# Performance work log

Hardware: AMD Instinct MI355X
Metric: run time of the kernel (lower is better)

The kernel has to match this reference:

```python
import jax, jax.numpy as jnp
import numpy as np


def setup_inputs() -> dict:
    key = jax.random.key(0)
    k1, k2 = jax.random.split(key)
    B, N, V = 8, 64, 128000
    sampled_probs = jax.random.uniform(k1, (B, N, V), dtype=jnp.float32)
    parent_probs = jax.random.uniform(k2, (B, N), dtype=jnp.float32)
    return {
        "sampled_probs": sampled_probs,
        "parent_probs": parent_probs,
        "sample_k": 64,
    }


def reference(sampled_probs, parent_probs, sample_k):
    # sampled_probs: [B, N, V] per-leaf next-token probs
    # parent_probs:  [B, N]    cumulative prob of each leaf (parent path)
    B, N, V = sampled_probs.shape
    # joint path probability: [B, N, V]
    global_probs = sampled_probs * parent_probs[:, :, None]
    # flatten leaves x vocab and take global top-k per batch row
    flattened = global_probs.reshape(B, N * V)
    topk_probs, topk_indices = jax.lax.top_k(flattened, sample_k)  # [B, k]
    # decode flat index -> (parent leaf index, token id)
    parent_indices = (topk_indices // V).astype(jnp.int64)
    token_ids = (topk_indices % V).astype(jnp.int64)
    return token_ids, topk_probs, parent_indices
```

## Files before the change

### kernel.cpp

```cpp
#include <hip/hip_runtime.h>
#include <stdint.h>

#define BATCH 8
#define NLEAF 64
#define VOCAB 128000
#define ROW (NLEAF * VOCAB)
#define CHUNK 4096
#define NCHUNK (ROW / CHUNK)
#define TOPK 64

__global__ __launch_bounds__(256) void k_chunkmax(
    const float* __restrict__ sp, const float* __restrict__ pp,
    float* __restrict__ cmax)
{
    int c   = blockIdx.x;
    int row = c / NCHUNK;
    int cr  = c - row * NCHUNK;
    long base = (long)row * ROW + (long)cr * CHUNK;
    int fr    = cr * CHUNK;
    int leaf0 = fr / VOCAB;
    int bnd   = (leaf0 + 1) * VOCAB;
    float p0  = pp[row * NLEAF + leaf0];
    float p1  = (leaf0 + 1 < NLEAF) ? pp[row * NLEAF + leaf0 + 1] : 0.f;

    int t = threadIdx.x;
    const float4* sp4 = (const float4*)(sp + base);
    float m = 0.f;
#pragma unroll
    for (int i = 0; i < 4; ++i) {
        int e4 = t + i * 256;
        float4 v = sp4[e4];
        float p = ((fr + e4 * 4) < bnd) ? p0 : p1;
        m = fmaxf(m, fmaxf(fmaxf(v.x * p, v.y * p), fmaxf(v.z * p, v.w * p)));
    }
    for (int off = 32; off; off >>= 1) m = fmaxf(m, __shfl_down(m, off, 64));
    __shared__ float s[4];
    if ((t & 63) == 0) s[t >> 6] = m;
    __syncthreads();
    if (t == 0) cmax[c] = fmaxf(fmaxf(s[0], s[1]), fmaxf(s[2], s[3]));
}

__global__ __launch_bounds__(256) void k_threshold(
    const float* __restrict__ cmax, float* __restrict__ thr,
    int* __restrict__ cnt)
{
    int row = blockIdx.x;
    int t = threadIdx.x;
    __shared__ unsigned uv[NCHUNK];
    __shared__ int hist[256], sc[256];
    __shared__ unsigned s_prefix;
    __shared__ int s_k;
    for (int i = t; i < NCHUNK; i += 256)
        uv[i] = __float_as_uint(cmax[row * NCHUNK + i]);
    if (t == 0) { cnt[row] = 0; s_prefix = 0u; s_k = TOPK; }
    __syncthreads();

    for (int level = 3; level >= 0; --level) {
        int shift = level * 8;
        hist[t] = 0;
        __syncthreads();
        unsigned prefix = s_prefix; int kk = s_k;
        for (int i = t; i < NCHUNK; i += 256) {
            unsigned u = uv[i];
            bool mm = (level == 3) || ((u >> (shift + 8)) == prefix);
            unsigned bin = mm ? ((u >> shift) & 255u) : 0xFFFFFFFFu;
            unsigned fb = __builtin_amdgcn_readfirstlane(bin);
            unsigned long long bal = __ballot(bin == fb);
            if (bal == ~0ull) {
                if ((t & 63) == 0 && fb != 0xFFFFFFFFu) atomicAdd(&hist[fb], 64);
            } else if (bin != 0xFFFFFFFFu) {
                atomicAdd(&hist[bin], 1);
            }
        }
        __syncthreads();
        sc[t] = hist[t];
        __syncthreads();
        for (int off = 1; off < 256; off <<= 1) {
            int v = sc[t];
            if (t + off < 256) v += sc[t + off];
            __syncthreads();
            sc[t] = v;
            __syncthreads();
        }
        int gt = (t < 255) ? sc[t + 1] : 0;
        if (gt < kk && kk <= gt + hist[t]) {
            s_prefix = (prefix << 8) | (unsigned)t;
            s_k = kk - gt;
        }
        __syncthreads();
    }
    if (t == 0) thr[row] = __uint_as_float(s_prefix);
}

__global__ __launch_bounds__(256) void k_collect(
    const float* __restrict__ sp, const float* __restrict__ pp,
    const float* __restrict__ cmax, const float* __restrict__ thr,
    int* __restrict__ cnt, unsigned long long* __restrict__ cand, int cap)
{
    int c   = blockIdx.x;
    int row = c / NCHUNK;
    float tval = thr[row];
    if (cmax[c] < tval) return;

    int cr = c - row * NCHUNK;
    long base = (long)row * ROW + (long)cr * CHUNK;
    int fr    = cr * CHUNK;
    int leaf0 = fr / VOCAB;
    int bnd   = (leaf0 + 1) * VOCAB;
    float p0  = pp[row * NLEAF + leaf0];
    float p1  = (leaf0 + 1 < NLEAF) ? pp[row * NLEAF + leaf0 + 1] : 0.f;

    int t = threadIdx.x;
    const float4* sp4 = (const float4*)(sp + base);
    float pr[16];
    int m = 0;
#pragma unroll
    for (int i = 0; i < 4; ++i) {
        int e4 = t + i * 256;
        float4 v = sp4[e4];
        float p = ((fr + e4 * 4) < bnd) ? p0 : p1;
        pr[i * 4 + 0] = v.x * p;
        pr[i * 4 + 1] = v.y * p;
        pr[i * 4 + 2] = v.z * p;
        pr[i * 4 + 3] = v.w * p;
#pragma unroll
        for (int j = 0; j < 4; ++j) m += (pr[i * 4 + j] >= tval) ? 1 : 0;
    }

    __shared__ int sc2[256];
    __shared__ int sbase;
    sc2[t] = m;
    __syncthreads();
    for (int off = 1; off < 256; off <<= 1) {
        int v = sc2[t];
        if (t >= off) v += sc2[t - off];
        __syncthreads();
        sc2[t] = v;
        __syncthreads();
    }
    if (t == 255) sbase = atomicAdd(&cnt[row], sc2[255]);
    __syncthreads();

    if (m > 0) {
        int pos = sbase + sc2[t] - m;
#pragma unroll
        for (int i = 0; i < 4; ++i) {
#pragma unroll
            for (int j = 0; j < 4; ++j) {
                float v = pr[i * 4 + j];
                if (v >= tval) {
                    if (pos < cap) {
                        unsigned fb = __float_as_uint(v);
                        unsigned fi = (unsigned)(fr + (t + i * 256) * 4 + j);
                        cand[(long)row * cap + pos] =
                            ((unsigned long long)fb << 32) |
                            (unsigned long long)(0xFFFFFFFFu - fi);
                    }
                    pos++;
                }
            }
        }
    }
}

__global__ __launch_bounds__(256) void k_final(
    const int* __restrict__ cnt, const unsigned long long* __restrict__ cand,
    int cap, float* __restrict__ out)
{
    int row = blockIdx.x;
    int t = threadIdx.x;
    int nc = cnt[row]; if (nc > cap) nc = cap;
    const unsigned long long* c = cand + (long)row * cap;

    __shared__ int hist[256], sc[256];
    __shared__ unsigned long long s_prefix;
    __shared__ int s_k;
    __shared__ unsigned long long stop[TOPK];
    __shared__ int s_ntop;
    if (t == 0) { s_prefix = 0ull; s_k = TOPK; s_ntop = 0; }
    __syncthreads();

    for (int level = 7; level >= 0; --level) {
        int shift = level * 8;
        hist[t] = 0;
        __syncthreads();
        unsigned long long prefix = s_prefix; int kk = s_k;
        for (int i = t; i < nc; i += 256) {
            unsigned long long u = c[i];
            bool mm = (level == 7) || ((u >> (shift + 8)) == prefix);
            unsigned bin = mm ? (unsigned)((u >> shift) & 255ull) : 0xFFFFFFFFu;
            unsigned fb = __builtin_amdgcn_readfirstlane(bin);
            unsigned long long bal = __ballot(bin == fb);
            if (bal == ~0ull) {
                if ((t & 63) == 0 && fb != 0xFFFFFFFFu) atomicAdd(&hist[fb], 64);
            } else if (bin != 0xFFFFFFFFu) {
                atomicAdd(&hist[bin], 1);
            }
        }
        __syncthreads();
        sc[t] = hist[t];
        __syncthreads();
        for (int off = 1; off < 256; off <<= 1) {
            int v = sc[t];
            if (t + off < 256) v += sc[t + off];
            __syncthreads();
            sc[t] = v;
            __syncthreads();
        }
        int gt = (t < 255) ? sc[t + 1] : 0;
        if (gt < kk && kk <= gt + hist[t]) {
            s_prefix = (prefix << 8) | (unsigned long long)t;
            s_k = kk - gt;
        }
        __syncthreads();
    }

    unsigned long long K64 = s_prefix;
    for (int i = t; i < nc; i += 256) {
        unsigned long long u = c[i];
        if (u >= K64) {
            int p = atomicAdd(&s_ntop, 1);
            if (p < TOPK) stop[p] = u;
        }
    }
    __syncthreads();

    int ntop = s_ntop; if (ntop > TOPK) ntop = TOPK;
    if (t < ntop) {
        unsigned long long mykey = stop[t];
        int rank = 0;
        for (int j = 0; j < ntop; ++j) rank += (stop[j] > mykey) ? 1 : 0;
        unsigned fi = 0xFFFFFFFFu - (unsigned)(mykey & 0xFFFFFFFFull);
        float val = __uint_as_float((unsigned)(mykey >> 32));
        int tok  = (int)(fi % VOCAB);
        int leaf = (int)(fi / VOCAB);
        out[row * TOPK + rank]                    = (float)tok;
        out[BATCH * TOPK + row * TOPK + rank]     = val;
        out[2 * BATCH * TOPK + row * TOPK + rank] = (float)leaf;
    }
}

extern "C" void kernel_launch(void* const* d_in, const int* in_sizes, int n_in,
                              void* d_out, int out_size, void* d_ws, size_t ws_size,
                              hipStream_t stream) {
    const float* sp = (const float*)d_in[0];
    const float* pp = (const float*)d_in[1];
    float* out = (float*)d_out;

    char* ws = (char*)d_ws;
    float* cmax = (float*)ws;
    float* thr  = (float*)(ws + 64000);
    int*   cnt  = (int*)(ws + 64032);
    unsigned long long* cand = (unsigned long long*)(ws + 65536);

    int cap = 16384;
    size_t need = 65536 + (size_t)BATCH * (size_t)cap * 8;
    if (ws_size < need) {
        cap = (int)((ws_size > 65536 ? (ws_size - 65536) : 0) / (BATCH * 8));
        if (cap < 256) cap = 256;
    }

    k_chunkmax <<<BATCH * NCHUNK, 256, 0, stream>>>(sp, pp, cmax);
    k_threshold<<<BATCH,          256, 0, stream>>>(cmax, thr, cnt);
    k_collect  <<<BATCH * NCHUNK, 256, 0, stream>>>(sp, pp, cmax, thr, cnt, cand, cap);
    k_final    <<<BATCH,          256, 0, stream>>>(cnt, cand, cap, out);
}
```

Before: 401.7 us.

## Compute per-512 sub-chunk maxima to tighten threshold and simplify leaf scaling

The chunk-max kernel now gives each 32-lane group one 512-element sub-chunk, which never crosses a leaf boundary. The parent probability becomes a single multiply after the max instead of a per-element select. The kernel writes both 512- and 4096-granularity maxima, and the threshold is found as the 64th largest of the finer 512-maxima, so it is tighter and the collect pass gathers far fewer candidates. The final kernel drops the ballot-based histogram fast path and uses plain atomics. The cost is a larger threshold pass (8x more entries to histogram), a bigger workspace, and narrower 32-lane access patterns.

```diff
diff --git a/kernel.cpp b/kernel.cpp
--- a/kernel.cpp
+++ b/kernel.cpp
@@ -7,51 +7,62 @@
 #define ROW (NLEAF * VOCAB)
 #define CHUNK 4096
 #define NCHUNK (ROW / CHUNK)
+#define SUB 512
+#define NSUB (ROW / SUB)
 #define TOPK 64
 
 __global__ __launch_bounds__(256) void k_chunkmax(
     const float* __restrict__ sp, const float* __restrict__ pp,
-    float* __restrict__ cmax)
+    float* __restrict__ cmax512, float* __restrict__ cmax4096)
 {
     int c   = blockIdx.x;
     int row = c / NCHUNK;
     int cr  = c - row * NCHUNK;
     long base = (long)row * ROW + (long)cr * CHUNK;
     int fr    = cr * CHUNK;
-    int leaf0 = fr / VOCAB;
-    int bnd   = (leaf0 + 1) * VOCAB;
-    float p0  = pp[row * NLEAF + leaf0];
-    float p1  = (leaf0 + 1 < NLEAF) ? pp[row * NLEAF + leaf0 + 1] : 0.f;
-
-    int t = threadIdx.x;
-    const float4* sp4 = (const float4*)(sp + base);
+
+    int t = threadIdx.x;
+    int g = t >> 5;
+    int l = t & 31;
+    int subfr = fr + g * SUB;
+    float p = pp[row * NLEAF + subfr / VOCAB];
+
+    const float4* sp4 = (const float4*)(sp + base + g * SUB);
     float m = 0.f;
 #pragma unroll
     for (int i = 0; i < 4; ++i) {
-        int e4 = t + i * 256;
-        float4 v = sp4[e4];
-        float p = ((fr + e4 * 4) < bnd) ? p0 : p1;
-        m = fmaxf(m, fmaxf(fmaxf(v.x * p, v.y * p), fmaxf(v.z * p, v.w * p)));
-    }
-    for (int off = 32; off; off >>= 1) m = fmaxf(m, __shfl_down(m, off, 64));
-    __shared__ float s[4];
-    if ((t & 63) == 0) s[t >> 6] = m;
-    __syncthreads();
-    if (t == 0) cmax[c] = fmaxf(fmaxf(s[0], s[1]), fmaxf(s[2], s[3]));
+        float4 v = sp4[l + i * 32];
+        m = fmaxf(m, fmaxf(fmaxf(v.x, v.y), fmaxf(v.z, v.w)));
+    }
+    for (int off = 16; off; off >>= 1) m = fmaxf(m, __shfl_down(m, off, 32));
+
+    __shared__ float s[8];
+    if (l == 0) {
+        float pm = p * m;
+        cmax512[(long)row * NSUB + cr * 8 + g] = pm;
+        s[g] = pm;
+    }
+    __syncthreads();
+    if (t == 0) {
+        float mm = s[0];
+#pragma unroll
+        for (int i = 1; i < 8; ++i) mm = fmaxf(mm, s[i]);
+        cmax4096[c] = mm;
+    }
 }
 
 __global__ __launch_bounds__(256) void k_threshold(
-    const float* __restrict__ cmax, float* __restrict__ thr,
+    const float* __restrict__ cmax512, float* __restrict__ thr,
     int* __restrict__ cnt)
 {
     int row = blockIdx.x;
     int t = threadIdx.x;
-    __shared__ unsigned uv[NCHUNK];
+    __shared__ unsigned uv[NSUB];
     __shared__ int hist[256], sc[256];
     __shared__ unsigned s_prefix;
     __shared__ int s_k;
-    for (int i = t; i < NCHUNK; i += 256)
-        uv[i] = __float_as_uint(cmax[row * NCHUNK + i]);
+    for (int i = t; i < NSUB; i += 256)
+        uv[i] = __float_as_uint(cmax512[(long)row * NSUB + i]);
     if (t == 0) { cnt[row] = 0; s_prefix = 0u; s_k = TOPK; }
     __syncthreads();
 
@@ -60,7 +71,7 @@
         hist[t] = 0;
         __syncthreads();
         unsigned prefix = s_prefix; int kk = s_k;
-        for (int i = t; i < NCHUNK; i += 256) {
+        for (int i = t; i < NSUB; i += 256) {
             unsigned u = uv[i];
             bool mm = (level == 3) || ((u >> (shift + 8)) == prefix);
             unsigned bin = mm ? ((u >> shift) & 255u) : 0xFFFFFFFFu;
@@ -94,31 +105,29 @@
 
 __global__ __launch_bounds__(256) void k_collect(
     const float* __restrict__ sp, const float* __restrict__ pp,
-    const float* __restrict__ cmax, const float* __restrict__ thr,
+    const float* __restrict__ cmax4096, const float* __restrict__ thr,
     int* __restrict__ cnt, unsigned long long* __restrict__ cand, int cap)
 {
     int c   = blockIdx.x;
     int row = c / NCHUNK;
     float tval = thr[row];
-    if (cmax[c] < tval) return;
+    if (cmax4096[c] < tval) return;
 
     int cr = c - row * NCHUNK;
     long base = (long)row * ROW + (long)cr * CHUNK;
     int fr    = cr * CHUNK;
-    int leaf0 = fr / VOCAB;
-    int bnd   = (leaf0 + 1) * VOCAB;
-    float p0  = pp[row * NLEAF + leaf0];
-    float p1  = (leaf0 + 1 < NLEAF) ? pp[row * NLEAF + leaf0 + 1] : 0.f;
-
-    int t = threadIdx.x;
-    const float4* sp4 = (const float4*)(sp + base);
+    int t = threadIdx.x;
+    int g = t >> 5;
+    int l = t & 31;
+    int subfr = fr + g * SUB;
+    float p = pp[row * NLEAF + subfr / VOCAB];
+
+    const float4* sp4 = (const float4*)(sp + base + g * SUB);
     float pr[16];
     int m = 0;
 #pragma unroll
     for (int i = 0; i < 4; ++i) {
-        int e4 = t + i * 256;
-        float4 v = sp4[e4];
-        float p = ((fr + e4 * 4) < bnd) ? p0 : p1;
+        float4 v = sp4[l + i * 32];
         pr[i * 4 + 0] = v.x * p;
         pr[i * 4 + 1] = v.y * p;
         pr[i * 4 + 2] = v.z * p;
@@ -151,7 +160,7 @@
                 if (v >= tval) {
                     if (pos < cap) {
                         unsigned fb = __float_as_uint(v);
-                        unsigned fi = (unsigned)(fr + (t + i * 256) * 4 + j);
+                        unsigned fi = (unsigned)(subfr + (l + i * 32) * 4 + j);
                         cand[(long)row * cap + pos] =
                             ((unsigned long long)fb << 32) |
                             (unsigned long long)(0xFFFFFFFFu - fi);
@@ -189,13 +198,7 @@
             unsigned long long u = c[i];
             bool mm = (level == 7) || ((u >> (shift + 8)) == prefix);
             unsigned bin = mm ? (unsigned)((u >> shift) & 255ull) : 0xFFFFFFFFu;
-            unsigned fb = __builtin_amdgcn_readfirstlane(bin);
-            unsigned long long bal = __ballot(bin == fb);
-            if (bal == ~0ull) {
-                if ((t & 63) == 0 && fb != 0xFFFFFFFFu) atomicAdd(&hist[fb], 64);
-            } else if (bin != 0xFFFFFFFFu) {
-                atomicAdd(&hist[bin], 1);
-            }
+            if (bin != 0xFFFFFFFFu) atomicAdd(&hist[bin], 1);
         }
         __syncthreads();
         sc[t] = hist[t];
@@ -248,20 +251,21 @@
     float* out = (float*)d_out;
 
     char* ws = (char*)d_ws;
-    float* cmax = (float*)ws;
-    float* thr  = (float*)(ws + 64000);
-    int*   cnt  = (int*)(ws + 64032);
-    unsigned long long* cand = (unsigned long long*)(ws + 65536);
+    float* cmax512  = (float*)ws;
+    float* cmax4096 = (float*)(ws + 512000);
+    float* thr      = (float*)(ws + 576000);
+    int*   cnt      = (int*)(ws + 576032);
+    unsigned long long* cand = (unsigned long long*)(ws + 589824);
 
     int cap = 16384;
-    size_t need = 65536 + (size_t)BATCH * (size_t)cap * 8;
+    size_t need = 589824 + (size_t)BATCH * (size_t)cap * 8;
     if (ws_size < need) {
-        cap = (int)((ws_size > 65536 ? (ws_size - 65536) : 0) / (BATCH * 8));
+        cap = (int)((ws_size > 589824 ? (ws_size - 589824) : 0) / (BATCH * 8));
         if (cap < 256) cap = 256;
     }
 
-    k_chunkmax <<<BATCH * NCHUNK, 256, 0, stream>>>(sp, pp, cmax);
-    k_threshold<<<BATCH,          256, 0, stream>>>(cmax, thr, cnt);
-    k_collect  <<<BATCH * NCHUNK, 256, 0, stream>>>(sp, pp, cmax, thr, cnt, cand, cap);
+    k_chunkmax <<<BATCH * NCHUNK, 256, 0, stream>>>(sp, pp, cmax512, cmax4096);
+    k_threshold<<<BATCH,          256, 0, stream>>>(cmax512, thr, cnt);
+    k_collect  <<<BATCH * NCHUNK, 256, 0, stream>>>(sp, pp, cmax4096, thr, cnt, cand, cap);
     k_final    <<<BATCH,          256, 0, stream>>>(cnt, cand, cap, out);
 }
```

After: 402.5 us. No clear change (+0.2%).
